# Optimization experiments

Measured on AMD Instinct MI355X. Metric: run time of the kernel, lower is better.

Reference implementation:

```python
import jax, jax.numpy as jnp
import numpy as np

HEAD_DIM = 128
HIDDEN = 5120
NUM_KV_GROUPS = 8
NUM_MODALITIES = 3
NUM_Q_HEADS = 40
QKV_PER_MOD = NUM_Q_HEADS * HEAD_DIM + 2 * NUM_KV_GROUPS * HEAD_DIM + NUM_Q_HEADS  # 7208


def _rms_norm(x, w, eps=1e-6):
    xf = x.astype(jnp.float32)
    inv = jax.lax.rsqrt(jnp.mean(xf * xf, axis=-1, keepdims=True) + eps)
    return (xf * inv).astype(x.dtype) * w


def _apply_rope(x, cos, sin):
    # x: [B,S,H,D], cos/sin: [B,S,rd]
    rd = cos.shape[-1]
    xr, xp = x[..., :rd], x[..., rd:]
    c, s = cos[:, :, None, :], sin[:, :, None, :]
    x1, x2 = xr[..., : rd // 2], xr[..., rd // 2:]
    rot = jnp.concatenate([-x2, x1], axis=-1)
    return jnp.concatenate([xr * c + rot * s, xp], axis=-1)


def setup_inputs() -> dict:
    key = jax.random.key(0)
    ks = jax.random.split(key, 6)
    B, S = 1, 2048
    return {
        "x": jax.random.normal(ks[0], (B, S, HIDDEN), jnp.float32),
        "rope_cos": jax.random.uniform(ks[1], (B, S, HEAD_DIM), jnp.float32),
        "rope_sin": jax.random.uniform(ks[2], (B, S, HEAD_DIM), jnp.float32),
        "modality_ids": jax.random.randint(ks[3], (B, S), 0, NUM_MODALITIES, jnp.int32),
        "pre_norm": jnp.ones((NUM_MODALITIES * HIDDEN,), jnp.float32),
        "qkv_w": jax.random.normal(ks[4], (NUM_MODALITIES * QKV_PER_MOD, HIDDEN), jnp.float32) * 0.02,
        "q_norm": jnp.ones((NUM_MODALITIES * HEAD_DIM,), jnp.float32),
        "k_norm": jnp.ones((NUM_MODALITIES * HEAD_DIM,), jnp.float32),
        "proj_w": jax.random.normal(ks[5], (NUM_MODALITIES * HIDDEN, HIDDEN), jnp.float32) * 0.02,
    }


def reference(x, rope_cos, rope_sin, modality_ids, pre_norm, qkv_w, q_norm, k_norm, proj_w):
    B, S, _ = x.shape
    # per-token modality gather of pre-norm weight
    norm_w = pre_norm.reshape(NUM_MODALITIES, HIDDEN)[modality_ids]  # [B,S,H]
    normed = _rms_norm(x, norm_w)

    # modality-routed QKV: compute all modalities, select with one-hot (dense, jit-friendly)
    oh = jax.nn.one_hot(modality_ids, NUM_MODALITIES, dtype=x.dtype)  # [B,S,M]
    qkv_w3 = qkv_w.reshape(NUM_MODALITIES, QKV_PER_MOD, HIDDEN)
    qkv_all = jnp.einsum("bsh,moh->bsmo", normed, qkv_w3)  # [B,S,M,QKV]
    qkv = jnp.einsum("bsm,bsmo->bso", oh, qkv_all)

    q_dim = NUM_Q_HEADS * HEAD_DIM
    k_dim = NUM_KV_GROUPS * HEAD_DIM
    q = qkv[..., :q_dim].reshape(B, S, NUM_Q_HEADS, HEAD_DIM)
    k = qkv[..., q_dim:q_dim + k_dim].reshape(B, S, NUM_KV_GROUPS, HEAD_DIM)
    v = qkv[..., q_dim + k_dim:q_dim + 2 * k_dim].reshape(B, S, NUM_KV_GROUPS, HEAD_DIM)
    gate = jax.nn.sigmoid(qkv[..., q_dim + 2 * k_dim:q_dim + 2 * k_dim + NUM_Q_HEADS])  # [B,S,NQ]

    qn = q_norm.reshape(NUM_MODALITIES, HEAD_DIM)[modality_ids][:, :, None, :]  # [B,S,1,D]
    kn = k_norm.reshape(NUM_MODALITIES, HEAD_DIM)[modality_ids][:, :, None, :]
    q = _rms_norm(q, qn)
    k = _rms_norm(k, kn)

    q = _apply_rope(q, rope_cos, rope_sin)
    k = _apply_rope(k, rope_cos, rope_sin)

    repeat = NUM_Q_HEADS // NUM_KV_GROUPS
    k = jnp.repeat(k, repeat, axis=2)  # [B,S,NQ,D]
    v = jnp.repeat(v, repeat, axis=2)

    scale = 1.0 / np.sqrt(HEAD_DIM)
    scores = jnp.einsum("bqhd,bkhd->bhqk", q, k) * scale  # [B,NQ,S,S]
    attn = jax.nn.softmax(scores, axis=-1)
    out = jnp.einsum("bhqk,bkhd->bqhd", attn, v)  # [B,S,NQ,D]

    out = (out * gate[..., None]).reshape(B, S, NUM_Q_HEADS * HEAD_DIM)

    proj_w3 = proj_w.reshape(NUM_MODALITIES, HIDDEN, HIDDEN)
    proj_all = jnp.einsum("bsh,moh->bsmo", out, proj_w3)  # [B,S,M,H]
    return jnp.einsum("bsm,bsmo->bso", oh, proj_all)
```

## Files before the change

kernel.cpp:

```cpp
#include <hip/hip_runtime.h>

typedef _Float16 f16;
typedef f16 f16x8 __attribute__((ext_vector_type(8)));
typedef f16 f16x4 __attribute__((ext_vector_type(4)));
typedef float f32x4 __attribute__((ext_vector_type(4)));

#define HID 5120
#define QKVO 7208
#define S_TOK 2048
#define NQH 40
#define NKV 8
#define HD 128

__device__ __forceinline__ void gload16(const void* g, void* l) {
    __builtin_amdgcn_global_load_lds(
        (const __attribute__((address_space(1))) void*)g,
        (__attribute__((address_space(3))) void*)l,
        16, 0, 0);
}

__global__ void sort_tokens(const int* __restrict__ mod, int* __restrict__ sorted,
                            int* __restrict__ offs)
{
    int tid = threadIdx.x, wave = tid >> 6, lane = tid & 63;
    int mloc[8];
    int c[3] = {0, 0, 0};
#pragma unroll
    for (int j = 0; j < 8; ++j) {
        int m = mod[tid * 8 + j];
        mloc[j] = m;
        c[m]++;
    }
    __shared__ int wsum[4][3];
    int excl[3];
#pragma unroll
    for (int m = 0; m < 3; ++m) {
        int v = c[m];
        int incl = v;
        for (int d = 1; d < 64; d <<= 1) {
            int n = __shfl_up(incl, d, 64);
            if (lane >= d) incl += n;
        }
        excl[m] = incl - v;
        if (lane == 63) wsum[wave][m] = incl;
    }
    __syncthreads();
    int wbase[3], tot[3];
#pragma unroll
    for (int m = 0; m < 3; ++m) {
        int b = 0, t = 0;
        for (int w = 0; w < 4; ++w) {
            if (w < wave) b += wsum[w][m];
            t += wsum[w][m];
        }
        wbase[m] = b;
        tot[m] = t;
    }
    int base[3];
    base[0] = 0;
    base[1] = tot[0];
    base[2] = tot[0] + tot[1];
    if (tid == 0) {
        offs[0] = 0;
        offs[1] = tot[0];
        offs[2] = tot[0] + tot[1];
        offs[3] = S_TOK;
    }
    int pos[3];
#pragma unroll
    for (int m = 0; m < 3; ++m) pos[m] = base[m] + wbase[m] + excl[m];
#pragma unroll
    for (int j = 0; j < 8; ++j) {
        int m = mloc[j];
        sorted[pos[m]++] = tid * 8 + j;
    }
}

__global__ void cvt_f32_f16(const float* __restrict__ src, f16* __restrict__ dst, int n4)
{
    int i = blockIdx.x * 256 + threadIdx.x;
    int stride = gridDim.x * 256;
    const float4* s4 = (const float4*)src;
    f16x4* d4 = (f16x4*)dst;
    for (; i < n4; i += stride) {
        float4 a = s4[i];
        f16x4 h;
        h[0] = (f16)a.x; h[1] = (f16)a.y; h[2] = (f16)a.z; h[3] = (f16)a.w;
        d4[i] = h;
    }
}

__global__ void rms_pre(const float* __restrict__ x, const int* __restrict__ mod,
                        const float* __restrict__ prenorm, f16* __restrict__ A1)
{
    int tok = blockIdx.x, tid = threadIdx.x;
    int m = mod[tok];
    const float4* xv = (const float4*)(x + (size_t)tok * HID);
    float4 v[5];
    float ss = 0.f;
#pragma unroll
    for (int j = 0; j < 5; ++j) {
        v[j] = xv[tid + 256 * j];
        ss += v[j].x * v[j].x + v[j].y * v[j].y + v[j].z * v[j].z + v[j].w * v[j].w;
    }
    for (int d = 1; d < 64; d <<= 1) ss += __shfl_xor(ss, d, 64);
    __shared__ float ws[4];
    if ((tid & 63) == 0) ws[tid >> 6] = ss;
    __syncthreads();
    float tot = ws[0] + ws[1] + ws[2] + ws[3];
    float inv = rsqrtf(tot * (1.f / HID) + 1e-6f);
    const float4* wv = (const float4*)(prenorm + (size_t)m * HID);
    f16x4* out4 = (f16x4*)(A1 + (size_t)tok * HID);
#pragma unroll
    for (int j = 0; j < 5; ++j) {
        float4 w = wv[tid + 256 * j];
        f16x4 h;
        h[0] = (f16)(v[j].x * inv * w.x);
        h[1] = (f16)(v[j].y * inv * w.y);
        h[2] = (f16)(v[j].z * inv * w.z);
        h[3] = (f16)(v[j].w * inv * w.w);
        out4[tid + 256 * j] = h;
    }
}

__global__ void gemm_grouped(const f16* __restrict__ A, const f16* __restrict__ W,
                             float* __restrict__ C,
                             const int* __restrict__ sorted_tok,
                             const int* __restrict__ mod_off, int NW, int NTN, int NPAN)
{
    const int K = HID;
    int F = blockIdx.x;
    int g = F & 7, s = F >> 3;
    int P = (s >> 4) * 8 + g;
    if (P >= NPAN) return;
    int mt = s & 15;
    int nt = P % NTN, mod = P / NTN;
    int off = mod_off[mod], cnt = mod_off[mod + 1] - off;
    if (mt * 128 >= cnt) return;
    __shared__ __align__(16) f16 As[128 * 64];
    __shared__ __align__(16) f16 Bs[128 * 64];
    __shared__ int rowtok[128];
    int tid = threadIdx.x, wave = tid >> 6, lane = tid & 63;
    if (tid < 128) {
        int r = mt * 128 + tid;
        rowtok[tid] = (r < cnt) ? sorted_tok[off + r] : -1;
    }
    __syncthreads();
    int wr = wave >> 1, wc = wave & 1;
    f32x4 acc[4][4] = {};
    const f16* Wm = W + (size_t)mod * NW * K;
    for (int kt = 0; kt < K / 64; ++kt) {
        int k0 = kt * 64;
#pragma unroll
        for (int it = 0; it < 4; ++it) {
            int c = it * 256 + tid;
            int row = c >> 3, kc = c & 7, skc = kc ^ (row & 7);
            int tk = rowtok[row];
            if (tk < 0) tk = 0;
            gload16(A + (size_t)tk * K + k0 + skc * 8, &As[c * 8]);
        }
#pragma unroll
        for (int it = 0; it < 4; ++it) {
            int c = it * 256 + tid;
            int row = c >> 3, kc = c & 7, skc = kc ^ (row & 7);
            int o = nt * 128 + row;
            if (o >= NW) o = NW - 1;
            gload16(Wm + (size_t)o * K + k0 + skc * 8, &Bs[c * 8]);
        }
        __syncthreads();
#pragma unroll
        for (int ks = 0; ks < 2; ++ks) {
            f16x8 a[4], b[4];
#pragma unroll
            for (int i = 0; i < 4; ++i) {
                int ar = wr * 64 + i * 16 + (lane & 15);
                int ac = (ks * 4 + (lane >> 4)) ^ (ar & 7);
                a[i] = *(const f16x8*)&As[ar * 64 + ac * 8];
                int br = wc * 64 + i * 16 + (lane & 15);
                int bc = (ks * 4 + (lane >> 4)) ^ (br & 7);
                b[i] = *(const f16x8*)&Bs[br * 64 + bc * 8];
            }
#pragma unroll
            for (int mi = 0; mi < 4; ++mi)
#pragma unroll
                for (int nj = 0; nj < 4; ++nj)
                    acc[mi][nj] = __builtin_amdgcn_mfma_f32_16x16x32_f16(
                        a[mi], b[nj], acc[mi][nj], 0, 0, 0);
        }
        __syncthreads();
    }
    int cl = lane & 15, rg = lane >> 4;
#pragma unroll
    for (int mi = 0; mi < 4; ++mi) {
#pragma unroll
        for (int rr = 0; rr < 4; ++rr) {
            int row = wr * 64 + mi * 16 + rg * 4 + rr;
            int tk = rowtok[row];
            if (tk < 0) continue;
            float* crow = C + (size_t)tk * NW;
#pragma unroll
            for (int nj = 0; nj < 4; ++nj) {
                int o = nt * 128 + wc * 64 + nj * 16 + cl;
                if (o < NW) crow[o] = acc[mi][nj][rr];
            }
        }
    }
}

__global__ void qkv_post(const float* __restrict__ qkv, const int* __restrict__ mod,
                         const float* __restrict__ cosb, const float* __restrict__ sinb,
                         const float* __restrict__ qnorm, const float* __restrict__ knorm,
                         f16* __restrict__ Qb, f16* __restrict__ Kb, float* __restrict__ gateb)
{
    int tok = blockIdx.x, tid = threadIdx.x;
    int wave = tid >> 6, lane = tid & 63;
    int m = mod[tok];
    float c0 = cosb[tok * HD + lane], c1 = cosb[tok * HD + 64 + lane];
    float s0 = sinb[tok * HD + lane], s1 = sinb[tok * HD + 64 + lane];
    const float* row = qkv + (size_t)tok * QKVO;
    for (int u = wave; u < 48; u += 4) {
        int base = (u < 40) ? u * HD : NQH * HD + (u - 40) * HD;
        float x0 = row[base + lane];
        float x1 = row[base + 64 + lane];
        float ss = x0 * x0 + x1 * x1;
        for (int d = 1; d < 64; d <<= 1) ss += __shfl_xor(ss, d, 64);
        float inv = rsqrtf(ss * (1.f / HD) + 1e-6f);
        const float* nw = (u < 40 ? qnorm : knorm) + m * HD;
        float n0 = x0 * inv * nw[lane];
        float n1 = x1 * inv * nw[64 + lane];
        float r0 = n0 * c0 - n1 * s0;
        float r1 = n1 * c1 + n0 * s1;
        if (u < 40) {
            const float sc = 0.08838834764831845f;
            r0 *= sc; r1 *= sc;
            Qb[((size_t)u * S_TOK + tok) * HD + lane] = (f16)r0;
            Qb[((size_t)u * S_TOK + tok) * HD + 64 + lane] = (f16)r1;
        } else {
            Kb[((size_t)(u - 40) * S_TOK + tok) * HD + lane] = (f16)r0;
            Kb[((size_t)(u - 40) * S_TOK + tok) * HD + 64 + lane] = (f16)r1;
        }
    }
    if (tid < 40) {
        float g = row[NQH * HD + 2 * NKV * HD + tid];
        gateb[tok * 40 + tid] = 1.f / (1.f + __expf(-g));
    }
}

__global__ void vtrans(const float* __restrict__ qkv, f16* __restrict__ Vt)
{
    int tc = blockIdx.x;
    int g = blockIdx.y;
    int tid = threadIdx.x;
    __shared__ float tile[64][129];
#pragma unroll
    for (int it = 0; it < 8; ++it) {
        int idx = it * 256 + tid;
        int r = idx >> 5, c4 = idx & 31;
        float4 v = *(const float4*)(qkv + (size_t)(tc * 64 + r) * QKVO + NQH * HD + NKV * HD + g * HD + c4 * 4);
        tile[r][c4 * 4 + 0] = v.x;
        tile[r][c4 * 4 + 1] = v.y;
        tile[r][c4 * 4 + 2] = v.z;
        tile[r][c4 * 4 + 3] = v.w;
    }
    __syncthreads();
    int d = tid >> 1, half = tid & 1;
    f16* dst = Vt + ((size_t)g * HD + d) * S_TOK + tc * 64 + half * 32;
#pragma unroll
    for (int j = 0; j < 32; ++j) dst[j] = (f16)tile[half * 32 + j][d];
}

__global__ void attn(const f16* __restrict__ Qb, const f16* __restrict__ Kb,
                     const f16* __restrict__ Vtb, const float* __restrict__ gateb,
                     f16* __restrict__ A2)
{
    int qt = blockIdx.x, h = blockIdx.y, grp = h / 5;
    int tid = threadIdx.x, wave = tid >> 6, lane = tid & 63;
    __shared__ __align__(16) f16 Qs[64 * 128];
    __shared__ __align__(16) f16 Ks[64 * 128];
    __shared__ __align__(16) f16 Vs[128 * 64];
    __shared__ __align__(16) f16 Ps[4][16 * 64];
    const f16* Qg = Qb + ((size_t)h * S_TOK + qt * 64) * HD;
#pragma unroll
    for (int it = 0; it < 4; ++it) {
        int c = it * 256 + tid, row = c >> 4, kc = c & 15, skc = kc ^ (row & 15);
        gload16(Qg + row * HD + skc * 8, &Qs[c * 8]);
    }
    __syncthreads();
    f16x8 qf[4];
    {
        int row = wave * 16 + (lane & 15);
#pragma unroll
        for (int ks = 0; ks < 4; ++ks) {
            int sk = (ks * 4 + (lane >> 4)) ^ (row & 15);
            qf[ks] = *(const f16x8*)&Qs[row * 128 + sk * 8];
        }
    }
    f32x4 o[8] = {};
    float mrow[4] = {-3.0e38f, -3.0e38f, -3.0e38f, -3.0e38f};
    float lrow[4] = {0.f, 0.f, 0.f, 0.f};
    const f16* Kg = Kb + (size_t)grp * S_TOK * HD;
    const f16* Vg = Vtb + (size_t)grp * HD * S_TOK;
    char* pbase = (char*)&Ps[wave][0];
    for (int t = 0; t < 32; ++t) {
#pragma unroll
        for (int it = 0; it < 4; ++it) {
            int c = it * 256 + tid, row = c >> 4, kc = c & 15, skc = kc ^ (row & 15);
            gload16(Kg + (size_t)(t * 64 + row) * HD + skc * 8, &Ks[c * 8]);
        }
#pragma unroll
        for (int it = 0; it < 4; ++it) {
            int c = it * 256 + tid, row = c >> 3, kc = c & 7, skc = kc ^ (row & 7);
            gload16(Vg + (size_t)row * S_TOK + t * 64 + skc * 8, &Vs[c * 8]);
        }
        __syncthreads();
        f32x4 s[4] = {};
#pragma unroll
        for (int ks = 0; ks < 4; ++ks) {
#pragma unroll
            for (int nj = 0; nj < 4; ++nj) {
                int kr = nj * 16 + (lane & 15);
                int sk = (ks * 4 + (lane >> 4)) ^ (kr & 15);
                f16x8 kf = *(const f16x8*)&Ks[kr * 128 + sk * 8];
                s[nj] = __builtin_amdgcn_mfma_f32_16x16x32_f16(qf[ks], kf, s[nj], 0, 0, 0);
            }
        }
        float mx[4], corr[4], psum[4];
#pragma unroll
        for (int r = 0; r < 4; ++r)
            mx[r] = fmaxf(fmaxf(s[0][r], s[1][r]), fmaxf(s[2][r], s[3][r]));
        for (int d = 1; d < 16; d <<= 1) {
#pragma unroll
            for (int r = 0; r < 4; ++r) mx[r] = fmaxf(mx[r], __shfl_xor(mx[r], d, 16));
        }
#pragma unroll
        for (int r = 0; r < 4; ++r) {
            float mn = fmaxf(mrow[r], mx[r]);
            corr[r] = __expf(mrow[r] - mn);
            mrow[r] = mn;
            psum[r] = 0.f;
        }
#pragma unroll
        for (int nj = 0; nj < 4; ++nj) {
#pragma unroll
            for (int r = 0; r < 4; ++r) {
                float p = __expf(s[nj][r] - mrow[r]);
                psum[r] += p;
                int prow = (lane >> 4) * 4 + r, col = (lane & 15) + nj * 16;
                int addr = (prow * 128 + col * 2) ^ ((prow & 7) << 4);
                *(f16*)(pbase + addr) = (f16)p;
            }
        }
        for (int d = 1; d < 16; d <<= 1) {
#pragma unroll
            for (int r = 0; r < 4; ++r) psum[r] += __shfl_xor(psum[r], d, 16);
        }
#pragma unroll
        for (int r = 0; r < 4; ++r) lrow[r] = lrow[r] * corr[r] + psum[r];
#pragma unroll
        for (int nj2 = 0; nj2 < 8; ++nj2)
#pragma unroll
            for (int r = 0; r < 4; ++r) o[nj2][r] *= corr[r];
#pragma unroll
        for (int ks2 = 0; ks2 < 2; ++ks2) {
            int prow = lane & 15;
            int sk = (ks2 * 4 + (lane >> 4)) ^ (prow & 7);
            f16x8 pa = *(const f16x8*)(pbase + prow * 128 + sk * 16);
#pragma unroll
            for (int nj2 = 0; nj2 < 8; ++nj2) {
                int vr = nj2 * 16 + (lane & 15);
                int skv = (ks2 * 4 + (lane >> 4)) ^ (vr & 7);
                f16x8 vf = *(const f16x8*)&Vs[vr * 64 + skv * 8];
                o[nj2] = __builtin_amdgcn_mfma_f32_16x16x32_f16(pa, vf, o[nj2], 0, 0, 0);
            }
        }
        __syncthreads();
    }
    int rbase = qt * 64 + wave * 16 + (lane >> 4) * 4;
#pragma unroll
    for (int r = 0; r < 4; ++r) {
        int tok = rbase + r;
        float sc = gateb[tok * 40 + h] / lrow[r];
#pragma unroll
        for (int nj2 = 0; nj2 < 8; ++nj2) {
            int d = nj2 * 16 + (lane & 15);
            A2[(size_t)tok * HID + h * HD + d] = (f16)(o[nj2][r] * sc);
        }
    }
}

extern "C" void kernel_launch(void* const* d_in, const int* in_sizes, int n_in,
                              void* d_out, int out_size, void* d_ws, size_t ws_size,
                              hipStream_t stream)
{
    const float* x = (const float*)d_in[0];
    const float* rc = (const float*)d_in[1];
    const float* rs = (const float*)d_in[2];
    const int* mod = (const int*)d_in[3];
    const float* prenorm = (const float*)d_in[4];
    const float* qkvw = (const float*)d_in[5];
    const float* qn = (const float*)d_in[6];
    const float* kn = (const float*)d_in[7];
    const float* projw = (const float*)d_in[8];
    float* out = (float*)d_out;

    char* p = (char*)d_ws;
    auto alloc = [&](size_t bytes) {
        char* r = p;
        p += (bytes + 255) & ~(size_t)255;
        return r;
    };
    int* sorted = (int*)alloc(S_TOK * 4);
    int* offs = (int*)alloc(16);
    f16* A1 = (f16*)alloc((size_t)S_TOK * HID * 2);
    f16* Wq = (f16*)alloc((size_t)3 * QKVO * HID * 2);
    f16* Wp = (f16*)alloc((size_t)3 * HID * HID * 2);
    float* qkv = (float*)alloc((size_t)S_TOK * QKVO * 4);
    f16* Qb = (f16*)alloc((size_t)NQH * S_TOK * HD * 2);
    f16* Kb = (f16*)alloc((size_t)NKV * S_TOK * HD * 2);
    f16* Vt = (f16*)alloc((size_t)NKV * HD * S_TOK * 2);
    float* gate = (float*)alloc((size_t)S_TOK * 40 * 4);
    f16* A2 = (f16*)alloc((size_t)S_TOK * HID * 2);
    if ((size_t)(p - (char*)d_ws) > ws_size) return;

    sort_tokens<<<1, 256, 0, stream>>>(mod, sorted, offs);
    cvt_f32_f16<<<2048, 256, 0, stream>>>(qkvw, Wq, 3 * QKVO * HID / 4);
    cvt_f32_f16<<<2048, 256, 0, stream>>>(projw, Wp, 3 * HID * HID / 4);
    rms_pre<<<2048, 256, 0, stream>>>(x, mod, prenorm, A1);
    {
        int NTN = 57, NPAN = NTN * 3;
        int grid = 8 * ((NPAN + 7) / 8) * 16;
        gemm_grouped<<<grid, 256, 0, stream>>>(A1, Wq, qkv, sorted, offs, QKVO, NTN, NPAN);
    }
    qkv_post<<<2048, 256, 0, stream>>>(qkv, mod, rc, rs, qn, kn, Qb, Kb, gate);
    vtrans<<<dim3(32, 8), 256, 0, stream>>>(qkv, Vt);
    attn<<<dim3(32, 40), 256, 0, stream>>>(Qb, Kb, Vt, gate, A2);
    {
        int NTN = 40, NPAN = NTN * 3;
        int grid = 8 * ((NPAN + 7) / 8) * 16;
        gemm_grouped<<<grid, 256, 0, stream>>>(A2, Wp, out, sorted, offs, HID, NTN, NPAN);
    }
}
```

Before: 926.3 us.

## Double-buffer K/V tiles in attention kernel with async prefetch

The attention kernel now keeps two LDS buffers for K and V and issues the global-to-LDS loads for the next tile before computing on the current one. The Q buffer region is reused as the second K buffer once Q has been moved into registers. Plain __syncthreads are replaced by manual vmcnt/lgkmcnt waits plus s_barrier, so load latency can overlap MFMA work. LDS use grows to 72KB, which may reduce how many blocks fit per CU, and the hand-written waitcnt values must match the exact count of outstanding loads.

```diff
diff --git a/kernel.cpp b/kernel.cpp
--- a/kernel.cpp
+++ b/kernel.cpp
@@ -275,17 +275,35 @@
 {
     int qt = blockIdx.x, h = blockIdx.y, grp = h / 5;
     int tid = threadIdx.x, wave = tid >> 6, lane = tid & 63;
-    __shared__ __align__(16) f16 Qs[64 * 128];
-    __shared__ __align__(16) f16 Ks[64 * 128];
-    __shared__ __align__(16) f16 Vs[128 * 64];
-    __shared__ __align__(16) f16 Ps[4][16 * 64];
+    __shared__ __align__(16) char smem[73728];
+    f16* Qs  = (f16*)smem;
+    f16* Kb0 = (f16*)(smem + 16384);
+    f16* Kb1 = (f16*)smem;
+    f16* Vb0 = (f16*)(smem + 32768);
+    f16* Vb1 = (f16*)(smem + 49152);
+    char* pbase = smem + 65536 + wave * 2048;
+
     const f16* Qg = Qb + ((size_t)h * S_TOK + qt * 64) * HD;
+    const f16* Kg = Kb + (size_t)grp * S_TOK * HD;
+    const f16* Vg = Vtb + (size_t)grp * HD * S_TOK;
+
 #pragma unroll
     for (int it = 0; it < 4; ++it) {
         int c = it * 256 + tid, row = c >> 4, kc = c & 15, skc = kc ^ (row & 15);
         gload16(Qg + row * HD + skc * 8, &Qs[c * 8]);
     }
-    __syncthreads();
+#pragma unroll
+    for (int it = 0; it < 4; ++it) {
+        int c = it * 256 + tid, row = c >> 4, kc = c & 15, skc = kc ^ (row & 15);
+        gload16(Kg + (size_t)row * HD + skc * 8, &Kb0[c * 8]);
+    }
+#pragma unroll
+    for (int it = 0; it < 4; ++it) {
+        int c = it * 256 + tid, row = c >> 3, kc = c & 7, skc = kc ^ (row & 7);
+        gload16(Vg + (size_t)row * S_TOK + skc * 8, &Vb0[c * 8]);
+    }
+    asm volatile("s_waitcnt vmcnt(8)" ::: "memory");
+    __builtin_amdgcn_s_barrier();
     f16x8 qf[4];
     {
         int row = wave * 16 + (lane & 15);
@@ -295,24 +313,36 @@
             qf[ks] = *(const f16x8*)&Qs[row * 128 + sk * 8];
         }
     }
+    asm volatile("s_waitcnt lgkmcnt(0)" ::: "memory");
+    __builtin_amdgcn_s_barrier();
+
     f32x4 o[8] = {};
     float mrow[4] = {-3.0e38f, -3.0e38f, -3.0e38f, -3.0e38f};
     float lrow[4] = {0.f, 0.f, 0.f, 0.f};
-    const f16* Kg = Kb + (size_t)grp * S_TOK * HD;
-    const f16* Vg = Vtb + (size_t)grp * HD * S_TOK;
-    char* pbase = (char*)&Ps[wave][0];
+
+    int cur = 0;
     for (int t = 0; t < 32; ++t) {
-#pragma unroll
-        for (int it = 0; it < 4; ++it) {
-            int c = it * 256 + tid, row = c >> 4, kc = c & 15, skc = kc ^ (row & 15);
-            gload16(Kg + (size_t)(t * 64 + row) * HD + skc * 8, &Ks[c * 8]);
-        }
-#pragma unroll
-        for (int it = 0; it < 4; ++it) {
-            int c = it * 256 + tid, row = c >> 3, kc = c & 7, skc = kc ^ (row & 7);
-            gload16(Vg + (size_t)row * S_TOK + t * 64 + skc * 8, &Vs[c * 8]);
-        }
-        __syncthreads();
+        f16* Ks = cur ? Kb1 : Kb0;
+        f16* Vs = cur ? Vb1 : Vb0;
+        if (t < 31) {
+            f16* Kn = cur ? Kb0 : Kb1;
+            f16* Vn = cur ? Vb0 : Vb1;
+#pragma unroll
+            for (int it = 0; it < 4; ++it) {
+                int c = it * 256 + tid, row = c >> 4, kc = c & 15, skc = kc ^ (row & 15);
+                gload16(Kg + (size_t)((t + 1) * 64 + row) * HD + skc * 8, &Kn[c * 8]);
+            }
+#pragma unroll
+            for (int it = 0; it < 4; ++it) {
+                int c = it * 256 + tid, row = c >> 3, kc = c & 7, skc = kc ^ (row & 7);
+                gload16(Vg + (size_t)row * S_TOK + (t + 1) * 64 + skc * 8, &Vn[c * 8]);
+            }
+            asm volatile("s_waitcnt vmcnt(8)" ::: "memory");
+        } else {
+            asm volatile("s_waitcnt vmcnt(0)" ::: "memory");
+        }
+        __builtin_amdgcn_s_barrier();
+
         f32x4 s[4] = {};
 #pragma unroll
         for (int ks = 0; ks < 4; ++ks) {
@@ -373,7 +403,9 @@
                 o[nj2] = __builtin_amdgcn_mfma_f32_16x16x32_f16(pa, vf, o[nj2], 0, 0, 0);
             }
         }
-        __syncthreads();
+        asm volatile("s_waitcnt lgkmcnt(0)" ::: "memory");
+        __builtin_amdgcn_s_barrier();
+        cur ^= 1;
     }
     int rbase = qt * 64 + wave * 16 + (lane >> 4) * 4;
 #pragma unroll
```

Result: no change. 914.0 us (-1.3%).
